# Kernel tuning notes

Hardware: AMD Instinct MI355X
Metric: run time of the kernel (lower is better)

Reference implementation:

```python
import jax, jax.numpy as jnp
import numpy as np

B, N, DIM = 2, 512, 512
H, DK, DV, PK, PV = 8, 16, 16, 4, 4
DPAIR = 128
NUM_LOGITS = 3  # scalar + point + pairwise
SCALAR_SCALE = (NUM_LOGITS * DK) ** -0.5
POINT_SCALE = ((NUM_LOGITS * PK) * (9.0 / 2.0)) ** -0.5
PAIR_SCALE = NUM_LOGITS ** -0.5
EPS = 1e-8
LN_EPS = 1e-3  # keras LayerNormalization default epsilon


def setup_inputs() -> dict:
    key = jax.random.key(0)
    ks = jax.random.split(key, 16)
    def rn(i, shape, s=0.02):
        return jax.random.normal(ks[i], shape, dtype=jnp.float32) * s
    f32 = jnp.float32
    return {
        "x": jax.random.normal(ks[0], (B, N, DIM), f32),
        "pairwise_repr": jax.random.normal(ks[1], (B, N, N, DPAIR), f32),
        "rotations": jax.random.normal(ks[2], (B, N, 3, 3), f32),
        "translations": jax.random.normal(ks[3], (B, N, 3), f32),
        "Wq_s": rn(4, (DIM, H * DK)),
        "Wk_s": rn(5, (DIM, H * DK)),
        "Wv_s": rn(6, (DIM, H * DV)),
        "Wq_p": rn(7, (DIM, H * PK * 3)),
        "Wk_p": rn(8, (DIM, H * PK * 3)),
        "Wv_p": rn(9, (DIM, H * PV * 3)),
        "point_weights": jnp.full((H,), float(np.log(np.exp(1.0) - 1.0)), f32),
        "Wpair": rn(10, (DPAIR, H)),
        "b_pair": jnp.zeros((H,), f32),
        "Wo": rn(11, (H * (DV + DPAIR + PV * 4), DIM)),
        "bo": jnp.zeros((DIM,), f32),
        "ln1_g": jnp.ones((DIM,), f32), "ln1_b": jnp.zeros((DIM,), f32),
        "ln2_g": jnp.ones((DIM,), f32), "ln2_b": jnp.zeros((DIM,), f32),
        "ff_w1": rn(12, (DIM, DIM)), "ff_b1": jnp.zeros((DIM,), f32),
        "ff_w2": rn(13, (DIM, DIM)), "ff_b2": jnp.zeros((DIM,), f32),
        "ff_w3": rn(14, (DIM, DIM)), "ff_b3": jnp.zeros((DIM,), f32),
    }


def _ln(x, g, b):
    m = jnp.mean(x, axis=-1, keepdims=True)
    v = jnp.mean(jnp.square(x - m), axis=-1, keepdims=True)
    return (x - m) * jax.lax.rsqrt(v + LN_EPS) * g + b


def _forward(x, pairwise_repr, rotations, translations,
             Wq_s, Wk_s, Wv_s, Wq_p, Wk_p, Wv_p, point_weights,
             Wpair, b_pair, Wo, bo, ln1_g, ln1_b, ln2_g, ln2_b,
             ff_w1, ff_b1, ff_w2, ff_b2, ff_w3, ff_b3):
    b, n, _ = x.shape
    # --- invariant point attention (post_norm=True -> attn sees raw x) ---
    qs = (x @ Wq_s).reshape(b, n, H, DK)
    ks = (x @ Wk_s).reshape(b, n, H, DK)
    vs = (x @ Wv_s).reshape(b, n, H, DV)

    t = translations[:, :, None, None, :]  # (b, n, 1, 1, 3)
    def to_global(w, p):
        pt = (x @ w).reshape(b, n, H, p, 3)  # local-frame points
        return jnp.einsum('bnhpc,bncr->bnhpr', pt, rotations) + t
    qp = to_global(Wq_p, PK)
    kp = to_global(Wk_p, PK)
    vp = to_global(Wv_p, PV)

    logits_s = jnp.einsum('bihd,bjhd->bhij', qs, ks) * SCALAR_SCALE
    logits_pair = (jnp.einsum('bijd,dh->bhij', pairwise_repr, Wpair)
                   + b_pair[None, :, None, None]) * PAIR_SCALE
    # point logits: -0.5 * w_h * scale * sum_{p,c} (q_i - k_j)^2,
    # expanded as q^2 + k^2 - 2qk to avoid a (b,i,j,h,p,3) intermediate
    w = 0.5 * jax.nn.softplus(point_weights) * POINT_SCALE  # (h,)
    q2w = jnp.einsum('bihp,h->bhi', jnp.square(qp).sum(-1), w)
    k2w = jnp.einsum('bjhp,h->bhj', jnp.square(kp).sum(-1), w)
    qkw = jnp.einsum('bihpc,bjhpc,h->bhij', qp, kp, w)
    logits_pt = 2.0 * qkw - q2w[:, :, :, None] - k2w[:, :, None, :]

    attn = jax.nn.softmax(logits_s + logits_pt + logits_pair, axis=-1)

    out_s = jnp.einsum('bhij,bjhd->bihd', attn, vs).reshape(b, n, H * DV)
    out_pair = jnp.einsum('bhij,bijd->bihd', attn, pairwise_repr).reshape(b, n, H * DPAIR)
    out_pg = jnp.einsum('bhij,bjhpc->bihpc', attn, vp)
    # map aggregated points back into each node's local frame: (g - t) @ R^T
    out_pl = jnp.einsum('bnhpr,bncr->bnhpc', out_pg - t, rotations)
    out_pn = jnp.sqrt(jnp.square(out_pl).sum(-1) + EPS)
    concat = jnp.concatenate([out_s,
                              out_pl.reshape(b, n, H * PV * 3),
                              out_pn.reshape(b, n, H * PV),
                              out_pair], axis=-1)
    attn_out = concat @ Wo + bo

    # --- residual + post-norm + FeedForward (3 dense layers, mult=1) ---
    a = _ln(attn_out + x, ln1_g, ln1_b)
    h1 = jax.nn.relu(a @ ff_w1 + ff_b1)
    h2 = jax.nn.relu(h1 @ ff_w2 + ff_b2)
    f = h2 @ ff_w3 + ff_b3
    return _ln(f + a, ln2_g, ln2_b)


def reference(x, pairwise_repr, rotations, translations,
              Wq_s, Wk_s, Wv_s, Wq_p, Wk_p, Wv_p, point_weights,
              Wpair, b_pair, Wo, bo, ln1_g, ln1_b, ln2_g, ln2_b,
              ff_w1, ff_b1, ff_w2, ff_b2, ff_w3, ff_b3):
    return _forward(x, pairwise_repr, rotations, translations,
                    Wq_s, Wk_s, Wv_s, Wq_p, Wk_p, Wv_p, point_weights,
                    Wpair, b_pair, Wo, bo, ln1_g, ln1_b, ln2_g, ln2_b,
                    ff_w1, ff_b1, ff_w2, ff_b2, ff_w3, ff_b3)
```

## Files before the change

### kernel.cpp

```cpp
#include <hip/hip_runtime.h>
#include <math.h>

#define Bb 2
#define Nn 512
#define RR 1024
#define HH 8
#define PROJC 704
#define CONCATC 1280
#define PSTRIDE 1280
#define NSPLIT 8
#define CH 64

#define SCALAR_SCALE 0.14433756729740643f
#define POINT_SCALE  0.13608276348795434f
#define PAIR_SCALE   0.5773502691896258f

typedef __attribute__((ext_vector_type(4))) float f32x4;
typedef __attribute__((ext_vector_type(8))) short short8;
typedef __attribute__((ext_vector_type(8))) unsigned short ush8;

__device__ __forceinline__ float wred_sum(float v) {
#pragma unroll
  for (int o = 1; o < 64; o <<= 1) v += __shfl_xor(v, o);
  return v;
}
__device__ __forceinline__ unsigned short f2bf(float f) {
  unsigned int u = __float_as_uint(f);
  unsigned int r = (u + 0x7FFFu + ((u >> 16) & 1u)) >> 16;
  return (unsigned short)r;
}

__global__ __launch_bounds__(256) void gather_wcat_t(
    const float* __restrict__ Wqs, const float* __restrict__ Wks,
    const float* __restrict__ Wvs, const float* __restrict__ Wqp,
    const float* __restrict__ Wkp, const float* __restrict__ Wvp,
    unsigned short* __restrict__ Wt) {
  int c = blockIdx.x;
  for (int k = threadIdx.x; k < 512; k += 256) {
    float val = 0.f;
    if (c < 128)      val = Wqs[k * 128 + c];
    else if (c < 256) val = Wks[k * 128 + c - 128];
    else if (c < 384) val = Wvs[k * 128 + c - 256];
    else if (c < 480) val = Wqp[k * 96 + c - 384];
    else if (c < 576) val = Wkp[k * 96 + c - 480];
    else if (c < 672) val = Wvp[k * 96 + c - 576];
    Wt[(size_t)c * 512 + k] = f2bf(val);
  }
}

__global__ __launch_bounds__(256) void transp_cvt4(
    const float* __restrict__ w0, const float* __restrict__ w1,
    const float* __restrict__ w2, const float* __restrict__ w3,
    unsigned short* __restrict__ o0, unsigned short* __restrict__ o1,
    unsigned short* __restrict__ o2, unsigned short* __restrict__ o3) {
  int z = blockIdx.z;
  const float* in = (z == 0) ? w0 : (z == 1) ? w1 : (z == 2) ? w2 : w3;
  unsigned short* out = (z == 0) ? o0 : (z == 1) ? o1 : (z == 2) ? o2 : o3;
  int K = (z == 0) ? 1280 : 512;
  int k0 = blockIdx.y * 32, n0 = blockIdx.x * 32;
  if (k0 >= K) return;
  __shared__ float tile[32][33];
  int t = threadIdx.x;
  int r = t >> 3, cq = (t & 7) * 4;
  float4 v = *(const float4*)&in[(size_t)(k0 + r) * 512 + n0 + cq];
  tile[r][cq] = v.x; tile[r][cq + 1] = v.y; tile[r][cq + 2] = v.z; tile[r][cq + 3] = v.w;
  __syncthreads();
  ushort4 o4;
  o4.x = f2bf(tile[cq + 0][r]);
  o4.y = f2bf(tile[cq + 1][r]);
  o4.z = f2bf(tile[cq + 2][r]);
  o4.w = f2bf(tile[cq + 3][r]);
  *(ushort4*)&out[(size_t)(n0 + r) * K + k0 + cq] = o4;
}

__global__ __launch_bounds__(256) void gemm_bf16_32(
    const float* __restrict__ A, int lda,
    const unsigned short* __restrict__ Bt, int K,
    float* __restrict__ C, int ldc,
    const float* __restrict__ bias, int relu) {
  __shared__ unsigned short As[32][72];
  __shared__ unsigned short Bs[64][72];
  int t = threadIdx.x;
  int lane = t & 63, w = t >> 6;
  int wc = w * 16;
  int fr = lane & 15, fk = (lane >> 4) * 8;
  f32x4 zero = {0.f, 0.f, 0.f, 0.f};
  f32x4 acc0 = zero, acc1 = zero;
  int bm = blockIdx.y * 32, bn = blockIdx.x * 64;
  int ar = t >> 3, ac = (t & 7) * 8;
  int br = t >> 2, bc = (t & 3) * 16;
  const float* Arow = A + (size_t)(bm + ar) * lda + ac;
  const unsigned short* Brow = Bt + (size_t)(bn + br) * K + bc;
  for (int k0 = 0; k0 < K; k0 += 64) {
    float4 a0 = *(const float4*)(Arow + k0);
    float4 a1 = *(const float4*)(Arow + k0 + 4);
    ush8 ap;
    ap[0] = f2bf(a0.x); ap[1] = f2bf(a0.y); ap[2] = f2bf(a0.z); ap[3] = f2bf(a0.w);
    ap[4] = f2bf(a1.x); ap[5] = f2bf(a1.y); ap[6] = f2bf(a1.z); ap[7] = f2bf(a1.w);
    ush8 b0 = *(const ush8*)(Brow + k0);
    ush8 b1 = *(const ush8*)(Brow + k0 + 8);
    *(ush8*)&As[ar][ac] = ap;
    *(ush8*)&Bs[br][bc] = b0;
    *(ush8*)&Bs[br][bc + 8] = b1;
    __syncthreads();
#pragma unroll
    for (int kk = 0; kk < 64; kk += 32) {
      short8 af0 = *(const short8*)&As[fr][kk + fk];
      short8 af1 = *(const short8*)&As[16 + fr][kk + fk];
      short8 bf = *(const short8*)&Bs[wc + fr][kk + fk];
      acc0 = __builtin_amdgcn_mfma_f32_16x16x32_bf16(af0, bf, acc0, 0, 0, 0);
      acc1 = __builtin_amdgcn_mfma_f32_16x16x32_bf16(af1, bf, acc1, 0, 0, 0);
    }
    __syncthreads();
  }
  int col = bn + wc + fr;
  float bv = bias ? bias[col] : 0.f;
#pragma unroll
  for (int mi = 0; mi < 2; mi++) {
    f32x4 av = (mi == 0) ? acc0 : acc1;
#pragma unroll
    for (int r = 0; r < 4; r++) {
      int row = bm + mi * 16 + (lane >> 4) * 4 + r;
      float v2 = av[r] + bv;
      if (relu) v2 = fmaxf(v2, 0.f);
      C[(size_t)row * ldc + col] = v2;
    }
  }
}

__global__ __launch_bounds__(128) void pointxform(
    const float* __restrict__ proj, const float* __restrict__ rot,
    const float* __restrict__ trans, float* __restrict__ qp,
    float* __restrict__ kp, float* __restrict__ vp) {
  int bn = blockIdx.x;
  int t = threadIdx.x;
  __shared__ float R[9];
  __shared__ float T[3];
  if (t < 9) R[t] = rot[bn * 9 + t];
  if (t < 3) T[t] = trans[bn * 3 + t];
  __syncthreads();
  if (t < 96) {
    int which = t >> 5;
    int pt = t & 31;
    const float* src = proj + (size_t)bn * PROJC + 384 + which * 96 + pt * 3;
    float c0 = src[0], c1 = src[1], c2 = src[2];
    float* dst = (which == 0 ? qp : (which == 1 ? kp : vp)) + (size_t)bn * 96 + pt * 3;
#pragma unroll
    for (int r = 0; r < 3; r++)
      dst[r] = c0 * R[0 * 3 + r] + c1 * R[1 * 3 + r] + c2 * R[2 * 3 + r] + T[r];
  }
}

__global__ __launch_bounds__(256) void flash_split(
    const float* __restrict__ pair, const float* __restrict__ Wpair,
    const float* __restrict__ proj, const float* __restrict__ qp,
    const float* __restrict__ kp, const float* __restrict__ vp,
    const float* __restrict__ pw, const float* __restrict__ b_pair,
    float* __restrict__ pbuf) {
  int bi = blockIdx.x, c = blockIdx.y;
  int b = bi >> 9;
  int j0 = c * CH;
  int t = threadIdx.x;
  __shared__ unsigned short pairN[64][136];
  __shared__ unsigned short WT[16][136];
  __shared__ unsigned short Pb[16][72];
  __shared__ float L[64][9];
  __shared__ float Pf[8][68];
  __shared__ float qs[128], qpi[96], wh[8], bp[8];
  __shared__ float msh[8], lsh[8];

  const float* pbase = pair + ((size_t)bi * 512 + j0) * 128;

#pragma unroll
  for (int it = 0; it < 8; it++) {
    int f = it * 256 + t;
    int j = f >> 5, dq = f & 31;
    float4 v = *(const float4*)&pbase[(size_t)j * 128 + dq * 4];
    ushort4 o;
    o.x = f2bf(v.x); o.y = f2bf(v.y); o.z = f2bf(v.z); o.w = f2bf(v.w);
    *(ushort4*)&pairN[j][dq * 4] = o;
  }
  if (t < 32) *(float4*)&qs[t * 4] = *(const float4*)&proj[(size_t)bi * PROJC + t * 4];
  if (t >= 32 && t < 56) *(float4*)&qpi[(t - 32) * 4] = *(const float4*)&qp[(size_t)bi * 96 + (t - 32) * 4];
  if (t >= 56 && t < 64) {
    wh[t - 56] = 0.5f * log1pf(__expf(pw[t - 56])) * POINT_SCALE;
    bp[t - 56] = b_pair[t - 56] * PAIR_SCALE;
  }
  if (t >= 64 && t < 192) {
    int d = t - 64;
    float4 a = *(const float4*)&Wpair[d * 8];
    float4 b2 = *(const float4*)&Wpair[d * 8 + 4];
    WT[0][d] = f2bf(a.x);  WT[1][d] = f2bf(a.y);
    WT[2][d] = f2bf(a.z);  WT[3][d] = f2bf(a.w);
    WT[4][d] = f2bf(b2.x); WT[5][d] = f2bf(b2.y);
    WT[6][d] = f2bf(b2.z); WT[7][d] = f2bf(b2.w);
  }
  {
    unsigned int* wz = (unsigned int*)&WT[8][0];
    for (int idx = t; idx < 8 * 68; idx += 256) wz[idx] = 0;
    unsigned int* pz = (unsigned int*)&Pb[8][0];
    for (int idx = t; idx < 8 * 36; idx += 256) pz[idx] = 0;
  }
  __syncthreads();

  {
    const float* kbase = proj + ((size_t)b * 512 + j0) * PROJC + 128;
    const float* kpbase = kp + ((size_t)b * 512 + j0) * 96;
    int h = t & 7;
#pragma unroll
    for (int r = 0; r < 2; r++) {
      int j = r * 32 + (t >> 3);
      const float* kr = kbase + (size_t)j * PROJC + h * 16;
      const float* kpr = kpbase + (size_t)j * 96 + h * 12;
      float s = 0.f;
#pragma unroll
      for (int dd = 0; dd < 16; dd++) s += qs[h * 16 + dd] * kr[dd];
      float d2 = 0.f;
#pragma unroll
      for (int p = 0; p < 12; p++) {
        float df = qpi[h * 12 + p] - kpr[p];
        d2 += df * df;
      }
      L[j][h] = s * SCALAR_SCALE - wh[h] * d2 + bp[h];
    }
  }
  __syncthreads();

  {
    int w = t >> 6, lane = t & 63;
    int fr = lane & 15, fko = (lane >> 4) * 8;
    f32x4 acc = {0.f, 0.f, 0.f, 0.f};
#pragma unroll
    for (int kk = 0; kk < 128; kk += 32) {
      short8 af = *(const short8*)&WT[fr][kk + fko];
      short8 bf = *(const short8*)&pairN[w * 16 + fr][kk + fko];
      acc = __builtin_amdgcn_mfma_f32_16x16x32_bf16(af, bf, acc, 0, 0, 0);
    }
    int row0 = (lane >> 4) * 4;
    if (row0 < 8) {
      int j = w * 16 + fr;
#pragma unroll
      for (int r = 0; r < 4; r++)
        L[j][row0 + r] += acc[r] * PAIR_SCALE;
    }
  }
  __syncthreads();

  if (t < 64) {
    int h = t >> 3, seg = t & 7;
    float m = -1e30f;
#pragma unroll
    for (int k = 0; k < 8; k++) m = fmaxf(m, L[seg * 8 + k][h]);
    m = fmaxf(m, __shfl_xor(m, 1));
    m = fmaxf(m, __shfl_xor(m, 2));
    m = fmaxf(m, __shfl_xor(m, 4));
    if (seg == 0) msh[h] = m;
  }
  __syncthreads();

  {
    int j = t & 63, w2 = t >> 6;
    int h0 = w2 * 2, h1 = h0 + 1;
    float p0 = __expf(L[j][h0] - msh[h0]);
    float p1 = __expf(L[j][h1] - msh[h1]);
    Pf[h0][j] = p0; Pf[h1][j] = p1;
    Pb[h0][j] = f2bf(p0); Pb[h1][j] = f2bf(p1);
    float s0 = wred_sum(p0);
    float s1 = wred_sum(p1);
    if (j == 0) { lsh[h0] = s0; lsh[h1] = s1; }
  }
  __syncthreads();

  float* po = pbuf + ((size_t)bi * NSPLIT + c) * PSTRIDE;

  {
    int lane = t & 63, w = t >> 6;
    int colm = lane & 15;
    int kgrp = (lane >> 4) * 8;
#pragma unroll
    for (int mi = 0; mi < 2; mi++) {
      int dt = w * 2 + mi;
      f32x4 acc = {0.f, 0.f, 0.f, 0.f};
#pragma unroll
      for (int kk = 0; kk < 64; kk += 32) {
        short8 af;
#pragma unroll
        for (int q = 0; q < 8; q++)
          af[q] = ((const short*)&pairN[kk + kgrp + q][0])[dt * 16 + colm];
        short8 bf = *(const short8*)&Pb[colm][kk + kgrp];
        acc = __builtin_amdgcn_mfma_f32_16x16x32_bf16(af, bf, acc, 0, 0, 0);
      }
      if (colm < 8) {
        int row0 = (lane >> 4) * 4;
#pragma unroll
        for (int r = 0; r < 4; r++)
          po[colm * 128 + dt * 16 + row0 + r] = acc[r];
      }
    }
  }

  float accs = 0.f, accg = 0.f;
  if (t < 128) {
    int hs = t >> 4;
    const float* vb = proj + ((size_t)b * 512 + j0) * PROJC + 256 + t;
#pragma unroll 8
    for (int j = 0; j < CH; j++) accs += Pf[hs][j] * vb[(size_t)j * PROJC];
    po[1024 + t] = accs;
  } else if (t < 224) {
    int ix = t - 128, hvv = ix / 12;
    const float* vb = vp + ((size_t)b * 512 + j0) * 96 + ix;
#pragma unroll 8
    for (int j = 0; j < CH; j++) accg += Pf[hvv][j] * vb[(size_t)j * 96];
    po[1152 + ix] = accg;
  }
  if (t < 8) { po[1248 + t] = msh[t]; po[1256 + t] = lsh[t]; }
}

__global__ __launch_bounds__(256) void combine_splits(
    const float* __restrict__ pbuf, const float* __restrict__ rot,
    const float* __restrict__ trans, float* __restrict__ concat) {
  int bi = blockIdx.x;
  int t = threadIdx.x;
  __shared__ float sc[NSPLIT][8];
  __shared__ float pg[96], plcl[96];
  __shared__ float Rm[9], Tv[3];
  if (t < 9) Rm[t] = rot[bi * 9 + t];
  if (t < 3) Tv[t] = trans[bi * 3 + t];
  const float* pb = pbuf + (size_t)bi * NSPLIT * PSTRIDE;
  if (t < 8) {
    float m[NSPLIT], lv[NSPLIT];
    float M = -1e30f;
#pragma unroll
    for (int cs = 0; cs < NSPLIT; cs++) {
      m[cs] = pb[cs * PSTRIDE + 1248 + t];
      lv[cs] = pb[cs * PSTRIDE + 1256 + t];
      M = fmaxf(M, m[cs]);
    }
    float D = 0.f, s[NSPLIT];
#pragma unroll
    for (int cs = 0; cs < NSPLIT; cs++) {
      s[cs] = __expf(m[cs] - M);
      D += lv[cs] * s[cs];
    }
    float inv = 1.f / D;
#pragma unroll
    for (int cs = 0; cs < NSPLIT; cs++) sc[cs][t] = s[cs] * inv;
  }
  __syncthreads();
  float* crow = concat + (size_t)bi * CONCATC;
#pragma unroll
  for (int q = 0; q < 4; q++) {
    int idx = q * 256 + t;
    int h = idx >> 7;
    float v = 0.f;
#pragma unroll
    for (int cs = 0; cs < NSPLIT; cs++) v += pb[cs * PSTRIDE + idx] * sc[cs][h];
    crow[256 + idx] = v;
  }
  if (t < 128) {
    int h = t >> 4;
    float v = 0.f;
#pragma unroll
    for (int cs = 0; cs < NSPLIT; cs++) v += pb[cs * PSTRIDE + 1024 + t] * sc[cs][h];
    crow[t] = v;
  } else if (t < 224) {
    int ix = t - 128, h = ix / 12;
    float v = 0.f;
#pragma unroll
    for (int cs = 0; cs < NSPLIT; cs++) v += pb[cs * PSTRIDE + 1152 + ix] * sc[cs][h];
    pg[ix] = v;
  }
  __syncthreads();
  if (t < 96) {
    int hp = t / 3, cc = t % 3;
    float v = 0.f;
#pragma unroll
    for (int r = 0; r < 3; r++) v += Rm[cc * 3 + r] * (pg[hp * 3 + r] - Tv[r]);
    plcl[t] = v;
    crow[128 + t] = v;
  }
  __syncthreads();
  if (t < 32) {
    float v0 = plcl[t * 3], v1 = plcl[t * 3 + 1], v2 = plcl[t * 3 + 2];
    crow[224 + t] = sqrtf(v0 * v0 + v1 * v1 + v2 * v2 + 1e-8f);
  }
}

__global__ __launch_bounds__(256) void ln_kernel(
    const float* __restrict__ in, const float* __restrict__ res,
    const float* __restrict__ g, const float* __restrict__ bt,
    float* __restrict__ out) {
  int row = blockIdx.x;
  int t = threadIdx.x;
  __shared__ float red[8];
  size_t base = (size_t)row * 512;
  float v0 = in[base + t] + res[base + t];
  float v1 = in[base + t + 256] + res[base + t + 256];
  int wid = t >> 6, lane = t & 63;
  float s = wred_sum(v0 + v1);
  if (lane == 0) red[wid] = s;
  __syncthreads();
  float mean = (red[0] + red[1] + red[2] + red[3]) * (1.f / 512.f);
  float d0 = v0 - mean, d1 = v1 - mean;
  float q = wred_sum(d0 * d0 + d1 * d1);
  __syncthreads();
  if (lane == 0) red[wid] = q;
  __syncthreads();
  float var = (red[0] + red[1] + red[2] + red[3]) * (1.f / 512.f);
  float rs = rsqrtf(var + 1e-3f);
  out[base + t] = d0 * rs * g[t] + bt[t];
  out[base + t + 256] = d1 * rs * g[t + 256] + bt[t + 256];
}

extern "C" void kernel_launch(void* const* d_in, const int* in_sizes, int n_in,
                              void* d_out, int out_size, void* d_ws, size_t ws_size,
                              hipStream_t stream) {
  const float* x      = (const float*)d_in[0];
  const float* pair   = (const float*)d_in[1];
  const float* rot    = (const float*)d_in[2];
  const float* trans  = (const float*)d_in[3];
  const float* Wqs    = (const float*)d_in[4];
  const float* Wks    = (const float*)d_in[5];
  const float* Wvs    = (const float*)d_in[6];
  const float* Wqp    = (const float*)d_in[7];
  const float* Wkp    = (const float*)d_in[8];
  const float* Wvp    = (const float*)d_in[9];
  const float* pw     = (const float*)d_in[10];
  const float* Wpair  = (const float*)d_in[11];
  const float* b_pair = (const float*)d_in[12];
  const float* Wo     = (const float*)d_in[13];
  const float* bo     = (const float*)d_in[14];
  const float* ln1g   = (const float*)d_in[15];
  const float* ln1b   = (const float*)d_in[16];
  const float* ln2g   = (const float*)d_in[17];
  const float* ln2b   = (const float*)d_in[18];
  const float* ffw1   = (const float*)d_in[19];
  const float* ffb1   = (const float*)d_in[20];
  const float* ffw2   = (const float*)d_in[21];
  const float* ffb2   = (const float*)d_in[22];
  const float* ffw3   = (const float*)d_in[23];
  const float* ffb3   = (const float*)d_in[24];
  float* out = (float*)d_out;

  float* ws = (float*)d_ws;
  unsigned short* Wcat_t = (unsigned short*)ws; ws += (704 * 512) / 2;
  unsigned short* Wo_t   = (unsigned short*)ws; ws += (512 * 1280) / 2;
  unsigned short* ff1_t  = (unsigned short*)ws; ws += (512 * 512) / 2;
  unsigned short* ff2_t  = (unsigned short*)ws; ws += (512 * 512) / 2;
  unsigned short* ff3_t  = (unsigned short*)ws; ws += (512 * 512) / 2;
  float* proj   = ws; ws += (size_t)RR * PROJC;
  float* qp     = ws; ws += RR * 96;
  float* kp     = ws; ws += RR * 96;
  float* vp     = ws; ws += RR * 96;
  float* pbuf   = ws; ws += (size_t)RR * NSPLIT * PSTRIDE;
  float* concat = ws; ws += (size_t)RR * CONCATC;
  float* tmp1   = ws; ws += RR * 512;
  float* a      = ws; ws += RR * 512;
  float* h1     = ws; ws += RR * 512;
  float* h2     = ws; ws += RR * 512;
  float* f      = ws; ws += RR * 512;

  dim3 b256(256);
  hipLaunchKernelGGL(gather_wcat_t, dim3(704), b256, 0, stream,
                     Wqs, Wks, Wvs, Wqp, Wkp, Wvp, Wcat_t);
  hipLaunchKernelGGL(transp_cvt4, dim3(16, 40, 4), b256, 0, stream,
                     Wo, ffw1, ffw2, ffw3, Wo_t, ff1_t, ff2_t, ff3_t);
  hipLaunchKernelGGL(gemm_bf16_32, dim3(11, 32), b256, 0, stream,
                     x, 512, Wcat_t, 512, proj, PROJC, (const float*)nullptr, 0);
  hipLaunchKernelGGL(pointxform, dim3(RR), dim3(128), 0, stream,
                     proj, rot, trans, qp, kp, vp);
  hipLaunchKernelGGL(flash_split, dim3(RR, NSPLIT), b256, 0, stream,
                     pair, Wpair, proj, qp, kp, vp, pw, b_pair, pbuf);
  hipLaunchKernelGGL(combine_splits, dim3(RR), b256, 0, stream,
                     pbuf, rot, trans, concat);
  hipLaunchKernelGGL(gemm_bf16_32, dim3(8, 32), b256, 0, stream,
                     concat, CONCATC, Wo_t, 1280, tmp1, 512, bo, 0);
  hipLaunchKernelGGL(ln_kernel, dim3(RR), b256, 0, stream, tmp1, x, ln1g, ln1b, a);
  hipLaunchKernelGGL(gemm_bf16_32, dim3(8, 32), b256, 0, stream,
                     a, 512, ff1_t, 512, h1, 512, ffb1, 1);
  hipLaunchKernelGGL(gemm_bf16_32, dim3(8, 32), b256, 0, stream,
                     h1, 512, ff2_t, 512, h2, 512, ffb2, 1);
  hipLaunchKernelGGL(gemm_bf16_32, dim3(8, 32), b256, 0, stream,
                     h2, 512, ff3_t, 512, f, 512, ffb3, 0);
  hipLaunchKernelGGL(ln_kernel, dim3(RR), b256, 0, stream, f, a, ln2g, ln2b, out);
}
```

Measured before the change: 175.8 us.

## Compute scalar value aggregation with MFMA and split point-value loop across threads

Replaces the scalar-value P·V loop, where 128 threads each read 64 strided fp32 values, with a bf16 MFMA. The V_s tile is reloaded into the pairN shared buffer and only the diagonal head block is kept. The point-value aggregation is split across 192 threads in two halves, combined through shared memory. The WT/Pb padding rows are removed by indexing with &7, which drops the zeroing loops. This adds extra syncs, a second global tile load, and bf16 rounding of V_s.

```diff
diff --git a/kernel.cpp b/kernel.cpp
--- a/kernel.cpp
+++ b/kernel.cpp
@@ -162,12 +162,13 @@
   int j0 = c * CH;
   int t = threadIdx.x;
   __shared__ unsigned short pairN[64][136];
-  __shared__ unsigned short WT[16][136];
-  __shared__ unsigned short Pb[16][72];
+  __shared__ unsigned short WT[8][136];
+  __shared__ unsigned short Pb[8][72];
   __shared__ float L[64][9];
   __shared__ float Pf[8][68];
   __shared__ float qs[128], qpi[96], wh[8], bp[8];
   __shared__ float msh[8], lsh[8];
+  __shared__ float pgpart[96];
 
   const float* pbase = pair + ((size_t)bi * 512 + j0) * 128;
 
@@ -195,12 +196,6 @@
     WT[4][d] = f2bf(b2.x); WT[5][d] = f2bf(b2.y);
     WT[6][d] = f2bf(b2.z); WT[7][d] = f2bf(b2.w);
   }
-  {
-    unsigned int* wz = (unsigned int*)&WT[8][0];
-    for (int idx = t; idx < 8 * 68; idx += 256) wz[idx] = 0;
-    unsigned int* pz = (unsigned int*)&Pb[8][0];
-    for (int idx = t; idx < 8 * 36; idx += 256) pz[idx] = 0;
-  }
   __syncthreads();
 
   {
@@ -232,7 +227,7 @@
     f32x4 acc = {0.f, 0.f, 0.f, 0.f};
 #pragma unroll
     for (int kk = 0; kk < 128; kk += 32) {
-      short8 af = *(const short8*)&WT[fr][kk + fko];
+      short8 af = *(const short8*)&WT[fr & 7][kk + fko];
       short8 bf = *(const short8*)&pairN[w * 16 + fr][kk + fko];
       acc = __builtin_amdgcn_mfma_f32_16x16x32_bf16(af, bf, acc, 0, 0, 0);
     }
@@ -287,7 +282,7 @@
 #pragma unroll
         for (int q = 0; q < 8; q++)
           af[q] = ((const short*)&pairN[kk + kgrp + q][0])[dt * 16 + colm];
-        short8 bf = *(const short8*)&Pb[colm][kk + kgrp];
+        short8 bf = *(const short8*)&Pb[colm & 7][kk + kgrp];
         acc = __builtin_amdgcn_mfma_f32_16x16x32_bf16(af, bf, acc, 0, 0, 0);
       }
       if (colm < 8) {
@@ -298,22 +293,59 @@
       }
     }
   }
-
-  float accs = 0.f, accg = 0.f;
-  if (t < 128) {
-    int hs = t >> 4;
-    const float* vb = proj + ((size_t)b * 512 + j0) * PROJC + 256 + t;
+  float accg = 0.f;
+  int ixg = (t < 96) ? t : t - 96;
+  if (t < 192) {
+    int jh = (t < 96) ? 0 : 1;
+    int hvv = ixg / 12;
+    const float* vb = vp + ((size_t)b * 512 + j0 + jh * 32) * 96 + ixg;
 #pragma unroll 8
-    for (int j = 0; j < CH; j++) accs += Pf[hs][j] * vb[(size_t)j * PROJC];
-    po[1024 + t] = accs;
-  } else if (t < 224) {
-    int ix = t - 128, hvv = ix / 12;
-    const float* vb = vp + ((size_t)b * 512 + j0) * 96 + ix;
-#pragma unroll 8
-    for (int j = 0; j < CH; j++) accg += Pf[hvv][j] * vb[(size_t)j * 96];
-    po[1152 + ix] = accg;
-  }
+    for (int j = 0; j < 32; j++) accg += Pf[hvv][jh * 32 + j] * vb[(size_t)j * 96];
+    if (t < 96) pgpart[ixg] = accg;
+  }
+  __syncthreads();
+
+  {
+    const float* vsb = proj + ((size_t)b * 512 + j0) * PROJC + 256;
+#pragma unroll
+    for (int it = 0; it < 8; it++) {
+      int f = it * 256 + t;
+      int j = f >> 5, dq = f & 31;
+      float4 v = *(const float4*)&vsb[(size_t)j * PROJC + dq * 4];
+      ushort4 o;
+      o.x = f2bf(v.x); o.y = f2bf(v.y); o.z = f2bf(v.z); o.w = f2bf(v.w);
+      *(ushort4*)&pairN[j][dq * 4] = o;
+    }
+  }
+  if (t >= 96 && t < 192) po[1152 + ixg] = pgpart[ixg] + accg;
   if (t < 8) { po[1248 + t] = msh[t]; po[1256 + t] = lsh[t]; }
+  __syncthreads();
+
+  {
+    int lane = t & 63, w = t >> 6;
+    int colm = lane & 15;
+    int kgrp = (lane >> 4) * 8;
+#pragma unroll
+    for (int mi = 0; mi < 2; mi++) {
+      int dt = w * 2 + mi;
+      f32x4 acc = {0.f, 0.f, 0.f, 0.f};
+#pragma unroll
+      for (int kk = 0; kk < 64; kk += 32) {
+        short8 af;
+#pragma unroll
+        for (int q = 0; q < 8; q++)
+          af[q] = ((const short*)&pairN[kk + kgrp + q][0])[dt * 16 + colm];
+        short8 bf = *(const short8*)&Pb[colm & 7][kk + kgrp];
+        acc = __builtin_amdgcn_mfma_f32_16x16x32_bf16(af, bf, acc, 0, 0, 0);
+      }
+      if (colm == dt) {
+        int row0 = (lane >> 4) * 4;
+#pragma unroll
+        for (int r = 0; r < 4; r++)
+          po[1024 + dt * 16 + row0 + r] = acc[r];
+      }
+    }
+  }
 }
 
 __global__ __launch_bounds__(256) void combine_splits(
```

Result: no change. 174.5 us (-0.8%).
